# Optimization experiments

Measured on AMD Instinct MI355X. Metric: run time of the kernel, lower is better.

## Reference

```python
import jax, jax.numpy as jnp
import numpy as np

EPS = 1e-5  # torch LayerNorm default


def setup_inputs() -> dict:
    key = jax.random.key(0)
    ks = jax.random.split(key, 4)
    B, S, D = 8, 1024, 768
    return {
        "q": jax.random.normal(ks[0], (B, S, D), dtype=jnp.float32),
        "k": jax.random.normal(ks[1], (B, S, D), dtype=jnp.float32),
        "v": jax.random.normal(ks[2], (B, S, D), dtype=jnp.float32),
        "W": jax.random.normal(ks[3], (D, D), dtype=jnp.float32) * (1.0 / np.sqrt(D)),
        "gamma": jnp.ones((D,), dtype=jnp.float32),
        "beta": jnp.zeros((D,), dtype=jnp.float32),
        "n_heads": 12,
    }


def reference(q, k, v, W, gamma, beta, n_heads):
    # Shapes: q,k,v [B,S,D]; W [D,D] (torch Linear weight, y = x @ W.T)
    B, S, D = q.shape
    Dh = D // n_heads

    proj = lambda x: jax.nn.relu(x @ W.T)
    q1, k1, v1 = proj(q), proj(k), proj(v)

    # chunk(dim=2) + cat(dim=0) == reshape to per-head [B,S,H,Dh]
    split = lambda x: x.reshape(B, S, n_heads, Dh)
    qh, kh, vh = split(q1), split(k1), split(v1)

    scale = 1.0 / (Dh ** 0.5)
    scores = jnp.einsum("bqhd,bkhd->bhqk", qh, kh) * scale  # [B,H,S,S]
    attn = jax.nn.softmax(scores, axis=-1)  # dropout is identity in eval mode
    out = jnp.einsum("bhqk,bkhd->bqhd", attn, vh).reshape(B, S, D)

    # `outputs += outputs + q` in torch -> outputs = 2*outputs + q
    out = 2.0 * out + q

    mu = jnp.mean(out, axis=-1, keepdims=True)
    var = jnp.var(out, axis=-1, keepdims=True)
    return (out - mu) / jnp.sqrt(var + EPS) * gamma + beta
```

## Files before the change

kernel.cpp:

```cpp
#include <hip/hip_runtime.h>
#include <hip/hip_bf16.h>

#define B_  8
#define S_  1024
#define D_  768
#define H_  12
#define DH_ 64

typedef __attribute__((ext_vector_type(8))) short bf16x8;
typedef __attribute__((ext_vector_type(4))) float f32x4;
typedef __attribute__((ext_vector_type(16))) float f32x16;

__device__ inline short f2bf(float f) {
    unsigned u = __builtin_bit_cast(unsigned, f);
    u = (u + 0x7fffu + ((u >> 16) & 1u)) >> 16;
    return (short)u;
}
__device__ inline float exp2_fast(float x) {
    float r; asm("v_exp_f32 %0, %1" : "=v"(r) : "v"(x)); return r;
}
__device__ inline unsigned cvt_pk_bf16(float lo, float hi) {
    unsigned r; asm("v_cvt_pk_bf16_f32 %0, %1, %2" : "=v"(r) : "v"(lo), "v"(hi)); return r;
}
__device__ inline float rcp_fast(float x) {
    float r; asm("v_rcp_f32 %0, %1" : "=v"(r) : "v"(x)); return r;
}
__device__ inline void plswap(unsigned& a, unsigned& b) {
    auto r = __builtin_amdgcn_permlane32_swap(a, b, false, false);
    a = r[0]; b = r[1];
}
__device__ inline float2 xhalves(float x) {
    unsigned u = __builtin_bit_cast(unsigned, x);
    auto r = __builtin_amdgcn_permlane32_swap(u, u, false, false);
    return make_float2(__builtin_bit_cast(float, r[0]),
                       __builtin_bit_cast(float, r[1]));
}
__device__ inline void gl_lds16(const void* gsrc, char* ldst) {
    __builtin_amdgcn_global_load_lds(
        (const __attribute__((address_space(1))) unsigned int*)gsrc,
        (__attribute__((address_space(3))) unsigned int*)ldst,
        16, 0, 0);
}

__global__ __launch_bounds__(256) void convw_kernel(
    const float* __restrict__ W, short* __restrict__ Wb)
{
    int i = (blockIdx.x * 256 + threadIdx.x) * 8;
    f32x4 a = *(const f32x4*)(W + i);
    f32x4 b = *(const f32x4*)(W + i + 4);
    uint4 pk;
    pk.x = cvt_pk_bf16(a[0], a[1]); pk.y = cvt_pk_bf16(a[2], a[3]);
    pk.z = cvt_pk_bf16(b[0], b[1]); pk.w = cvt_pk_bf16(b[2], b[3]);
    *(uint4*)(Wb + i) = pk;
}

__global__ __launch_bounds__(512) void proj_kernel(
    const float* __restrict__ q, const float* __restrict__ k,
    const float* __restrict__ v, const short* __restrict__ Wb,
    short* __restrict__ q1, short* __restrict__ k1, short* __restrict__ v1t)
{
    __shared__ __align__(16) char lds[65536];

    int p  = blockIdx.x;
    int L  = (p & 7) * 96 + (p >> 3);
    int mt = L >> 1, nb = L & 1;
    int t  = mt >> 7;
    int m0 = (mt & 127) << 6;
    int n0 = nb * 384;
    const float* X = (t == 0) ? q : (t == 1) ? k : v;

    int tid = threadIdx.x, lane = tid & 63, w = tid >> 6;
    int l15 = lane & 15, g = lane >> 4;

    int xrow = w * 8 + (lane >> 3), xc = lane & 7;
    const float* xsrc = X + (size_t)(m0 + xrow) * D_ + ((xc ^ (xrow & 7)) << 2);
    char* xdst = lds + w * 1024;
    int wrow0 = w * 48 + (lane >> 2), wc = lane & 3;
    int wrow1 = wrow0 + 16, wrow2 = wrow0 + 32;
    const short* wsrc0 = Wb + (size_t)(n0 + wrow0) * D_ + ((wc ^ ((wrow0 >> 1) & 3)) << 3);
    const short* wsrc1 = Wb + (size_t)(n0 + wrow1) * D_ + ((wc ^ ((wrow1 >> 1) & 3)) << 3);
    const short* wsrc2 = Wb + (size_t)(n0 + wrow2) * D_ + ((wc ^ ((wrow2 >> 1) & 3)) << 3);
    char* wdst = lds + 16384 + w * 3072;

#define ISSUE(s_, b_) do { int _ko = (s_) * 32; \
        gl_lds16(xsrc + _ko, xdst + (b_) * 8192); \
        gl_lds16(wsrc0 + _ko, wdst + (b_) * 24576); \
        gl_lds16(wsrc1 + _ko, wdst + (b_) * 24576 + 1024); \
        gl_lds16(wsrc2 + _ko, wdst + (b_) * 24576 + 2048); \
    } while (0)

    f32x4 acc[4][3];
    #pragma unroll
    for (int m = 0; m < 4; m++)
        #pragma unroll
        for (int n = 0; n < 3; n++) acc[m][n] = (f32x4){0.f, 0.f, 0.f, 0.f};

    ISSUE(0, 0);
    for (int s = 0; s < 24; ++s) {
        __builtin_amdgcn_s_barrier();
        asm volatile("" ::: "memory");
        if (s + 1 < 24) {
            ISSUE(s + 1, (s + 1) & 1);
            asm volatile("s_waitcnt vmcnt(4)" ::: "memory");
        } else {
            asm volatile("s_waitcnt vmcnt(0)" ::: "memory");
        }
        __builtin_amdgcn_s_barrier();
        asm volatile("" ::: "memory");

        const char* Xb = lds + (s & 1) * 8192;
        const char* Wp = lds + 16384 + (s & 1) * 24576;
        bf16x8 af[4];
        #pragma unroll
        for (int m = 0; m < 4; m++) {
            int r = m * 16 + l15;
            const char* rp = Xb + r * 128;
            f32x4 lo = *(const f32x4*)(rp + (((2 * g)     ^ (r & 7)) << 4));
            f32x4 hi = *(const f32x4*)(rp + (((2 * g + 1) ^ (r & 7)) << 4));
            uint4 pk;
            pk.x = cvt_pk_bf16(lo[0], lo[1]); pk.y = cvt_pk_bf16(lo[2], lo[3]);
            pk.z = cvt_pk_bf16(hi[0], hi[1]); pk.w = cvt_pk_bf16(hi[2], hi[3]);
            af[m] = __builtin_bit_cast(bf16x8, pk);
        }
        bf16x8 bfv[3];
        #pragma unroll
        for (int n = 0; n < 3; n++) {
            int r = w * 48 + n * 16 + l15;
            bfv[n] = *(const bf16x8*)(Wp + r * 64 + ((g ^ ((r >> 1) & 3)) << 4));
        }
        __builtin_amdgcn_s_setprio(1);
        #pragma unroll
        for (int m = 0; m < 4; m++)
            #pragma unroll
            for (int n = 0; n < 3; n++)
                acc[m][n] = __builtin_amdgcn_mfma_f32_16x16x32_bf16(
                    af[m], bfv[n], acc[m][n], 0, 0, 0);
        __builtin_amdgcn_s_setprio(0);
    }
#undef ISSUE

    __syncthreads();
    const float sc1 = (t == 1) ? 0.18033688011112793f : 1.0f;
    #pragma unroll
    for (int m = 0; m < 4; m++)
        #pragma unroll
        for (int n = 0; n < 3; n++)
            #pragma unroll
            for (int r = 0; r < 4; r++) {
                int row = m * 16 + g * 4 + r;
                int col = w * 48 + n * 16 + l15;
                short vv = f2bf(fmaxf(acc[m][n][r], 0.f) * sc1);
                if (t == 2)
                    *(short*)(lds + col * 128 + (((row >> 3) ^ (col & 7)) << 4)
                              + ((row & 7) << 1)) = vv;
                else
                    *(short*)(lds + row * 768 + (((col >> 3) ^ (row & 7)) << 4)
                              + ((col & 7) << 1)) = vv;
            }
    __syncthreads();
    int bb2 = m0 >> 10;
    if (t == 2) {
        #pragma unroll
        for (int j = 0; j < 6; j++) {
            int c = tid * 6 + j;
            int vr = c >> 3, ch = c & 7;
            bf16x8 val = *(const bf16x8*)(lds + vr * 128 + ((ch ^ (vr & 7)) << 4));
            int gc = n0 + vr, h = gc >> 6, dh = gc & 63;
            *(bf16x8*)(v1t + (((size_t)bb2 * H_ + h) * DH_ + dh) * S_
                       + (m0 & 1023) + ch * 8) = val;
        }
    } else {
        short* dst0 = t ? k1 : q1;
        #pragma unroll
        for (int j = 0; j < 6; j++) {
            int c = tid * 6 + j;
            int row = c / 48, ch = c % 48;
            bf16x8 val = *(const bf16x8*)(lds + row * 768 + ((ch ^ (row & 7)) << 4));
            int m = m0 + row, ss = m & 1023;
            int gc = n0 + ch * 8, h = gc >> 6, dh = gc & 63;
            *(bf16x8*)(dst0 + (((size_t)bb2 * H_ + h) * S_ + ss) * DH_ + dh) = val;
        }
    }
}

__global__ __launch_bounds__(256, 3) void attn_kernel(
    const short* __restrict__ q1, const short* __restrict__ k1,
    const short* __restrict__ v1t, float* __restrict__ out)
{
    __shared__ short Klds[2][4096];
    __shared__ short Vlds[2][4096];
    __shared__ float lsum_lds[4][32];

    int d    = blockIdx.x;
    int head = (d & 7) + ((d >> 6) << 3);
    int qi   = (d >> 3) & 7;
    int bb   = head / H_, hh = head % H_;

    int tid = threadIdx.x, lane = tid & 63, w = tid >> 6;
    int l31 = lane & 31, hi = lane >> 5;
    int qbase = (qi * 4 + w) * 32;

    const short* Qp = q1  + (size_t)head * S_ * DH_;
    const short* Kp = k1  + (size_t)head * S_ * DH_;
    const short* Vp = v1t + (size_t)head * DH_ * S_;

    int sr = tid >> 2, sc = tid & 3;
    int swz0 = sr * 128 + ((sc       ^ (sr & 7)) << 4);
    int swz1 = sr * 128 + (((sc + 4) ^ (sr & 7)) << 4);

    bf16x8 stK0, stK1, stV0, stV1;

#define LOADST(kvb) do { \
        const short* _kg = Kp + (size_t)((kvb) + sr) * DH_; \
        const short* _vg = Vp + (size_t)sr * S_ + (kvb); \
        stK0 = *(const bf16x8*)(_kg + sc * 8); \
        stK1 = *(const bf16x8*)(_kg + (sc + 4) * 8); \
        stV0 = *(const bf16x8*)(_vg + sc * 8); \
        stV1 = *(const bf16x8*)(_vg + (sc + 4) * 8); \
    } while (0)
#define WRITEST(buf) do { \
        char* _kb = (char*)&Klds[buf][0]; \
        char* _vb = (char*)&Vlds[buf][0]; \
        *(bf16x8*)(_kb + swz0) = stK0; \
        *(bf16x8*)(_kb + swz1) = stK1; \
        *(bf16x8*)(_vb + swz0) = stV0; \
        *(bf16x8*)(_vb + swz1) = stV1; \
    } while (0)

    bf16x8 qf[4];
    #pragma unroll
    for (int kb = 0; kb < 4; kb++)
        qf[kb] = *(const bf16x8*)(Qp + (size_t)(qbase + l31) * DH_ + kb * 16 + hi * 8);

    f32x16 o0, o1;
    #pragma unroll
    for (int r = 0; r < 16; r++) { o0[r] = 0.f; o1[r] = 0.f; }
    float mreg = -1e30f, lsum = 0.f;

    int xk = l31 & 7;

    auto subtile = [&](int cur, int j) {
        const char* Kt = (const char*)&Klds[cur][0];
        const char* Vt = (const char*)&Vlds[cur][0];
        int rK = (32 * j + l31) * 128;
        bf16x8 kf0 = *(const bf16x8*)(Kt + rK + (((0 + hi) ^ xk) << 4));
        bf16x8 kf1 = *(const bf16x8*)(Kt + rK + (((2 + hi) ^ xk) << 4));
        bf16x8 kf2 = *(const bf16x8*)(Kt + rK + (((4 + hi) ^ xk) << 4));
        bf16x8 kf3 = *(const bf16x8*)(Kt + rK + (((6 + hi) ^ xk) << 4));
        int rV0 = l31 * 128, rV1 = (32 + l31) * 128;
        int s0 = ((4 * j + hi) ^ xk) << 4, s1 = ((4 * j + 2 + hi) ^ xk) << 4;
        bf16x8 vf00 = *(const bf16x8*)(Vt + rV0 + s0);
        bf16x8 vf01 = *(const bf16x8*)(Vt + rV0 + s1);
        bf16x8 vf10 = *(const bf16x8*)(Vt + rV1 + s0);
        bf16x8 vf11 = *(const bf16x8*)(Vt + rV1 + s1);

        f32x16 s;
        #pragma unroll
        for (int r = 0; r < 16; r++) s[r] = 0.f;
        __builtin_amdgcn_s_setprio(1);
        s = __builtin_amdgcn_mfma_f32_32x32x16_bf16(kf0, qf[0], s, 0, 0, 0);
        s = __builtin_amdgcn_mfma_f32_32x32x16_bf16(kf1, qf[1], s, 0, 0, 0);
        s = __builtin_amdgcn_mfma_f32_32x32x16_bf16(kf2, qf[2], s, 0, 0, 0);
        s = __builtin_amdgcn_mfma_f32_32x32x16_bf16(kf3, qf[3], s, 0, 0, 0);
        __builtin_amdgcn_s_setprio(0);

        float t0 = fmaxf(s[0], s[1]),   t1 = fmaxf(s[2], s[3]);
        float t2 = fmaxf(s[4], s[5]),   t3 = fmaxf(s[6], s[7]);
        float t4 = fmaxf(s[8], s[9]),   t5 = fmaxf(s[10], s[11]);
        float t6 = fmaxf(s[12], s[13]), t7 = fmaxf(s[14], s[15]);
        float u0 = fmaxf(t0, t1), u1 = fmaxf(t2, t3);
        float u2 = fmaxf(t4, t5), u3 = fmaxf(t6, t7);
        float pmax = fmaxf(fmaxf(u0, u1), fmaxf(u2, u3));
        float2 ph = xhalves(pmax);
        pmax = fmaxf(ph.x, ph.y);

        if (!__all(pmax <= mreg + 8.f)) {
            float mn = fmaxf(mreg, pmax);
            float sc_ = exp2_fast(mreg - mn);
            mreg = mn; lsum *= sc_;
            if (hi == 0) lsum_lds[w][l31] = sc_;
            asm volatile("s_waitcnt lgkmcnt(0)" ::: "memory");
            #pragma unroll
            for (int r = 0; r < 16; r++) {
                int crow = (r & 3) + ((r >> 2) << 3) + (hi << 2);
                float srw = lsum_lds[w][crow];
                o0[r] *= srw; o1[r] *= srw;
            }
        }

        #pragma unroll
        for (int r = 0; r < 16; r++) s[r] = exp2_fast(s[r] - mreg);

        float a0 = s[0] + s[1],   a1 = s[2] + s[3];
        float a2 = s[4] + s[5],   a3 = s[6] + s[7];
        float a4 = s[8] + s[9],   a5 = s[10] + s[11];
        float a6 = s[12] + s[13], a7 = s[14] + s[15];
        float rsum = ((a0 + a1) + (a2 + a3)) + ((a4 + a5) + (a6 + a7));
        float2 rh = xhalves(rsum);
        lsum += rh.x + rh.y;

        unsigned c0 = cvt_pk_bf16(s[0], s[1]);
        unsigned c1 = cvt_pk_bf16(s[2], s[3]);
        unsigned c2 = cvt_pk_bf16(s[4], s[5]);
        unsigned c3 = cvt_pk_bf16(s[6], s[7]);
        unsigned c4 = cvt_pk_bf16(s[8], s[9]);
        unsigned c5 = cvt_pk_bf16(s[10], s[11]);
        unsigned c6 = cvt_pk_bf16(s[12], s[13]);
        unsigned c7 = cvt_pk_bf16(s[14], s[15]);
        plswap(c0, c2);
        plswap(c1, c3);
        plswap(c4, c6);
        plswap(c5, c7);

        union U { unsigned u[4]; bf16x8 v; };
        U f0, f1;
        f0.u[0] = c0; f0.u[1] = c1; f0.u[2] = c2; f0.u[3] = c3;
        f1.u[0] = c4; f1.u[1] = c5; f1.u[2] = c6; f1.u[3] = c7;

        __builtin_amdgcn_s_setprio(1);
        o0 = __builtin_amdgcn_mfma_f32_32x32x16_bf16(f0.v, vf00, o0, 0, 0, 0);
        o0 = __builtin_amdgcn_mfma_f32_32x32x16_bf16(f1.v, vf01, o0, 0, 0, 0);
        o1 = __builtin_amdgcn_mfma_f32_32x32x16_bf16(f0.v, vf10, o1, 0, 0, 0);
        o1 = __builtin_amdgcn_mfma_f32_32x32x16_bf16(f1.v, vf11, o1, 0, 0, 0);
        __builtin_amdgcn_s_setprio(0);
    };

    LOADST(0);
    WRITEST(0);
    LOADST(64);
    asm volatile("s_waitcnt lgkmcnt(0)" ::: "memory");
    __builtin_amdgcn_s_barrier();
    asm volatile("" ::: "memory");

    int cur = 0;
    for (int t = 0; t < 16; t++) {
        if (t < 15) {
            WRITEST(cur ^ 1);
            if (t < 14) LOADST((t + 2) * 64);
        }
        subtile(cur, 0);
        subtile(cur, 1);
        if (t < 15) {
            asm volatile("" ::: "memory");
            asm volatile("s_waitcnt lgkmcnt(0)" ::: "memory");
            __builtin_amdgcn_s_barrier();
            asm volatile("" ::: "memory");
        }
        cur ^= 1;
    }
#undef LOADST
#undef WRITEST

    if (hi == 0) lsum_lds[w][l31] = lsum;
    asm volatile("s_waitcnt lgkmcnt(0)" ::: "memory");
    #pragma unroll
    for (int r = 0; r < 16; r++) {
        int crow = (r & 3) + ((r >> 2) << 3) + (hi << 2);
        float inv = rcp_fast(lsum_lds[w][crow]);
        float* op = out + ((size_t)(bb * S_ + qbase + crow)) * D_ + hh * DH_ + l31;
        op[0]  = o0[r] * inv;
        op[32] = o1[r] * inv;
    }
}

__global__ __launch_bounds__(192) void ln_kernel(
    const float* __restrict__ qin, const float* __restrict__ gamma,
    const float* __restrict__ beta, float* __restrict__ out)
{
    int row = blockIdx.x;
    int tid = threadIdx.x;
    size_t base = (size_t)row * D_ + tid * 4;

    f32x4 o  = *(const f32x4*)(out + base);
    f32x4 qv = *(const f32x4*)(qin + base);
    f32x4 x;
    float sum = 0.f, sq = 0.f;
    #pragma unroll
    for (int i = 0; i < 4; i++) {
        x[i] = 2.f * o[i] + qv[i];
        sum += x[i];
        sq  += x[i] * x[i];
    }
    #pragma unroll
    for (int msk = 1; msk < 64; msk <<= 1) {
        sum += __shfl_xor(sum, msk);
        sq  += __shfl_xor(sq, msk);
    }
    __shared__ float s1[3], s2[3];
    if ((tid & 63) == 0) { s1[tid >> 6] = sum; s2[tid >> 6] = sq; }
    __syncthreads();
    sum = s1[0] + s1[1] + s1[2];
    sq  = s2[0] + s2[1] + s2[2];
    float mu   = sum * (1.f / D_);
    float var  = sq * (1.f / D_) - mu * mu;
    float rstd = rsqrtf(var + 1e-5f);
    f32x4 g = *(const f32x4*)(gamma + tid * 4);
    f32x4 b = *(const f32x4*)(beta + tid * 4);
    f32x4 y;
    #pragma unroll
    for (int i = 0; i < 4; i++)
        y[i] = (x[i] - mu) * rstd * g[i] + b[i];
    *(f32x4*)(out + base) = y;
}

extern "C" void kernel_launch(void* const* d_in, const int* in_sizes, int n_in,
                              void* d_out, int out_size, void* d_ws, size_t ws_size,
                              hipStream_t stream)
{
    const float* q     = (const float*)d_in[0];
    const float* k     = (const float*)d_in[1];
    const float* v     = (const float*)d_in[2];
    const float* W     = (const float*)d_in[3];
    const float* gamma = (const float*)d_in[4];
    const float* beta  = (const float*)d_in[5];

    size_t per = (size_t)B_ * H_ * S_ * DH_;
    short* q1  = (short*)d_ws;
    short* k1  = q1 + per;
    short* v1t = k1 + per;
    short* Wb  = v1t + per;
    float* out = (float*)d_out;

    convw_kernel<<<dim3(288), dim3(256), 0, stream>>>(W, Wb);
    proj_kernel<<<dim3(768), dim3(512), 0, stream>>>(q, k, v, Wb, q1, k1, v1t);
    attn_kernel<<<dim3(768), dim3(256), 0, stream>>>(q1, k1, v1t, out);
    ln_kernel<<<dim3(B_ * S_), dim3(192), 0, stream>>>(q, gamma, beta, out);
}
```

Measured before the change: 117.5 us.

## Retile projection GEMM to 128x256 tiles with register-staged bf16 A conversion

The projection GEMM moves from 64x384 tiles with 512 threads to 128x256 tiles with 256 threads, where each wave computes a 64x128 sub-tile (4x8 MFMA accumulators). The fp32 activations are now loaded into registers one step ahead, converted to bf16 once, and written to LDS. Previously every k-step read fp32 from LDS and converted it inside the MFMA loop. The loop uses a single barrier per iteration. The aim is more MFMA work per LDS read, less conversion work, and fewer barriers, at the cost of more accumulator registers and fewer blocks (576).

```diff
diff --git a/kernel.cpp b/kernel.cpp
--- a/kernel.cpp
+++ b/kernel.cpp
@@ -54,7 +54,7 @@
     *(uint4*)(Wb + i) = pk;
 }
 
-__global__ __launch_bounds__(512) void proj_kernel(
+__global__ __launch_bounds__(256) void proj_kernel(
     const float* __restrict__ q, const float* __restrict__ k,
     const float* __restrict__ v, const short* __restrict__ Wb,
     short* __restrict__ q1, short* __restrict__ k1, short* __restrict__ v1t)
@@ -62,122 +62,145 @@
     __shared__ __align__(16) char lds[65536];
 
     int p  = blockIdx.x;
-    int L  = (p & 7) * 96 + (p >> 3);
-    int mt = L >> 1, nb = L & 1;
-    int t  = mt >> 7;
-    int m0 = (mt & 127) << 6;
-    int n0 = nb * 384;
+    int L  = (p & 7) * 72 + (p >> 3);
+    int mt = L / 3, nt = L % 3;
+    int t  = mt >> 6;
+    int m0 = (mt & 63) << 7;
+    int n0 = nt << 8;
     const float* X = (t == 0) ? q : (t == 1) ? k : v;
 
     int tid = threadIdx.x, lane = tid & 63, w = tid >> 6;
+    int wr = w >> 1, wc = w & 1;
     int l15 = lane & 15, g = lane >> 4;
 
-    int xrow = w * 8 + (lane >> 3), xc = lane & 7;
-    const float* xsrc = X + (size_t)(m0 + xrow) * D_ + ((xc ^ (xrow & 7)) << 2);
-    char* xdst = lds + w * 1024;
-    int wrow0 = w * 48 + (lane >> 2), wc = lane & 3;
-    int wrow1 = wrow0 + 16, wrow2 = wrow0 + 32;
-    const short* wsrc0 = Wb + (size_t)(n0 + wrow0) * D_ + ((wc ^ ((wrow0 >> 1) & 3)) << 3);
-    const short* wsrc1 = Wb + (size_t)(n0 + wrow1) * D_ + ((wc ^ ((wrow1 >> 1) & 3)) << 3);
-    const short* wsrc2 = Wb + (size_t)(n0 + wrow2) * D_ + ((wc ^ ((wrow2 >> 1) & 3)) << 3);
-    char* wdst = lds + 16384 + w * 3072;
-
-#define ISSUE(s_, b_) do { int _ko = (s_) * 32; \
-        gl_lds16(xsrc + _ko, xdst + (b_) * 8192); \
-        gl_lds16(wsrc0 + _ko, wdst + (b_) * 24576); \
-        gl_lds16(wsrc1 + _ko, wdst + (b_) * 24576 + 1024); \
-        gl_lds16(wsrc2 + _ko, wdst + (b_) * 24576 + 2048); \
+    int tr = tid >> 1, ch = tid & 1;
+    const float* asrc = X + (size_t)(m0 + tr) * D_ + ch * 16;
+    int awb0 = tr * 64 + (((2 * ch)     ^ ((tr >> 1) & 3)) << 4);
+    int awb1 = tr * 64 + (((2 * ch + 1) ^ ((tr >> 1) & 3)) << 4);
+
+    const short* bsrc[4];
+    int bofs[4];
+    #pragma unroll
+    for (int i = 0; i < 4; i++) {
+        int r = w * 64 + i * 16 + (lane >> 2);
+        int c = lane & 3;
+        bsrc[i] = Wb + (size_t)(n0 + r) * D_ + ((c ^ ((r >> 1) & 3)) << 3);
+        bofs[i] = (w * 64 + i * 16) * 64;
+    }
+
+    f32x4 pf[4];
+#define LOADA(s_) do { \
+        pf[0] = *(const f32x4*)(asrc + (s_) * 32); \
+        pf[1] = *(const f32x4*)(asrc + (s_) * 32 + 4); \
+        pf[2] = *(const f32x4*)(asrc + (s_) * 32 + 8); \
+        pf[3] = *(const f32x4*)(asrc + (s_) * 32 + 12); \
     } while (0)
-
-    f32x4 acc[4][3];
+#define ISSUE_B(s_, b_) do { \
+        _Pragma("unroll") \
+        for (int i = 0; i < 4; i++) \
+            gl_lds16(bsrc[i] + (s_) * 32, lds + (b_) * 24576 + 8192 + bofs[i]); \
+    } while (0)
+#define CVT_WRITE_A(b_) do { \
+        uint4 u0, u1; \
+        u0.x = cvt_pk_bf16(pf[0][0], pf[0][1]); u0.y = cvt_pk_bf16(pf[0][2], pf[0][3]); \
+        u0.z = cvt_pk_bf16(pf[1][0], pf[1][1]); u0.w = cvt_pk_bf16(pf[1][2], pf[1][3]); \
+        u1.x = cvt_pk_bf16(pf[2][0], pf[2][1]); u1.y = cvt_pk_bf16(pf[2][2], pf[2][3]); \
+        u1.z = cvt_pk_bf16(pf[3][0], pf[3][1]); u1.w = cvt_pk_bf16(pf[3][2], pf[3][3]); \
+        *(uint4*)(lds + (b_) * 24576 + awb0) = u0; \
+        *(uint4*)(lds + (b_) * 24576 + awb1) = u1; \
+    } while (0)
+
+    f32x4 acc[4][8];
     #pragma unroll
     for (int m = 0; m < 4; m++)
         #pragma unroll
-        for (int n = 0; n < 3; n++) acc[m][n] = (f32x4){0.f, 0.f, 0.f, 0.f};
-
-    ISSUE(0, 0);
+        for (int n = 0; n < 8; n++) acc[m][n] = (f32x4){0.f, 0.f, 0.f, 0.f};
+
+    LOADA(0);
+    ISSUE_B(0, 0);
+    CVT_WRITE_A(0);
+    LOADA(1);
+    asm volatile("s_waitcnt vmcnt(4) lgkmcnt(0)" ::: "memory");
+    __builtin_amdgcn_s_barrier();
+    asm volatile("" ::: "memory");
+
+    #pragma unroll 2
     for (int s = 0; s < 24; ++s) {
-        __builtin_amdgcn_s_barrier();
-        asm volatile("" ::: "memory");
+        const char* Ab = lds + (s & 1) * 24576;
+        const char* Bb = Ab + 8192;
+        bf16x8 af[4];
+        #pragma unroll
+        for (int m = 0; m < 4; m++) {
+            int ra = wr * 64 + m * 16 + l15;
+            af[m] = *(const bf16x8*)(Ab + ra * 64 + ((g ^ ((ra >> 1) & 3)) << 4));
+        }
+        __builtin_amdgcn_s_setprio(1);
+        #pragma unroll
+        for (int n = 0; n < 8; n++) {
+            int rb = wc * 128 + n * 16 + l15;
+            bf16x8 bv = *(const bf16x8*)(Bb + rb * 64 + ((g ^ ((rb >> 1) & 3)) << 4));
+            #pragma unroll
+            for (int m = 0; m < 4; m++)
+                acc[m][n] = __builtin_amdgcn_mfma_f32_16x16x32_bf16(
+                    af[m], bv, acc[m][n], 0, 0, 0);
+        }
+        __builtin_amdgcn_s_setprio(0);
+
         if (s + 1 < 24) {
-            ISSUE(s + 1, (s + 1) & 1);
-            asm volatile("s_waitcnt vmcnt(4)" ::: "memory");
-        } else {
-            asm volatile("s_waitcnt vmcnt(0)" ::: "memory");
-        }
-        __builtin_amdgcn_s_barrier();
-        asm volatile("" ::: "memory");
-
-        const char* Xb = lds + (s & 1) * 8192;
-        const char* Wp = lds + 16384 + (s & 1) * 24576;
-        bf16x8 af[4];
-        #pragma unroll
-        for (int m = 0; m < 4; m++) {
-            int r = m * 16 + l15;
-            const char* rp = Xb + r * 128;
-            f32x4 lo = *(const f32x4*)(rp + (((2 * g)     ^ (r & 7)) << 4));
-            f32x4 hi = *(const f32x4*)(rp + (((2 * g + 1) ^ (r & 7)) << 4));
-            uint4 pk;
-            pk.x = cvt_pk_bf16(lo[0], lo[1]); pk.y = cvt_pk_bf16(lo[2], lo[3]);
-            pk.z = cvt_pk_bf16(hi[0], hi[1]); pk.w = cvt_pk_bf16(hi[2], hi[3]);
-            af[m] = __builtin_bit_cast(bf16x8, pk);
-        }
-        bf16x8 bfv[3];
-        #pragma unroll
-        for (int n = 0; n < 3; n++) {
-            int r = w * 48 + n * 16 + l15;
-            bfv[n] = *(const bf16x8*)(Wp + r * 64 + ((g ^ ((r >> 1) & 3)) << 4));
-        }
-        __builtin_amdgcn_s_setprio(1);
-        #pragma unroll
-        for (int m = 0; m < 4; m++)
-            #pragma unroll
-            for (int n = 0; n < 3; n++)
-                acc[m][n] = __builtin_amdgcn_mfma_f32_16x16x32_bf16(
-                    af[m], bfv[n], acc[m][n], 0, 0, 0);
-        __builtin_amdgcn_s_setprio(0);
-    }
-#undef ISSUE
+            ISSUE_B(s + 1, (s + 1) & 1);
+            CVT_WRITE_A((s + 1) & 1);
+            if (s + 2 < 24) {
+                LOADA(s + 2);
+                asm volatile("s_waitcnt vmcnt(4) lgkmcnt(0)" ::: "memory");
+            } else {
+                asm volatile("s_waitcnt vmcnt(0) lgkmcnt(0)" ::: "memory");
+            }
+            __builtin_amdgcn_s_barrier();
+            asm volatile("" ::: "memory");
+        }
+    }
+#undef LOADA
+#undef ISSUE_B
+#undef CVT_WRITE_A
 
     __syncthreads();
     const float sc1 = (t == 1) ? 0.18033688011112793f : 1.0f;
     #pragma unroll
     for (int m = 0; m < 4; m++)
         #pragma unroll
-        for (int n = 0; n < 3; n++)
+        for (int n = 0; n < 8; n++)
             #pragma unroll
             for (int r = 0; r < 4; r++) {
-                int row = m * 16 + g * 4 + r;
-                int col = w * 48 + n * 16 + l15;
+                int row = wr * 64 + m * 16 + g * 4 + r;
+                int col = wc * 128 + n * 16 + l15;
                 short vv = f2bf(fmaxf(acc[m][n][r], 0.f) * sc1);
                 if (t == 2)
-                    *(short*)(lds + col * 128 + (((row >> 3) ^ (col & 7)) << 4)
+                    *(short*)(lds + col * 256 + (((row >> 3) ^ (col & 15)) << 4)
                               + ((row & 7) << 1)) = vv;
                 else
-                    *(short*)(lds + row * 768 + (((col >> 3) ^ (row & 7)) << 4)
+                    *(short*)(lds + row * 512 + (((col >> 3) ^ (row & 31)) << 4)
                               + ((col & 7) << 1)) = vv;
             }
     __syncthreads();
     int bb2 = m0 >> 10;
     if (t == 2) {
-        #pragma unroll
-        for (int j = 0; j < 6; j++) {
-            int c = tid * 6 + j;
-            int vr = c >> 3, ch = c & 7;
-            bf16x8 val = *(const bf16x8*)(lds + vr * 128 + ((ch ^ (vr & 7)) << 4));
-            int gc = n0 + vr, h = gc >> 6, dh = gc & 63;
-            *(bf16x8*)(v1t + (((size_t)bb2 * H_ + h) * DH_ + dh) * S_
-                       + (m0 & 1023) + ch * 8) = val;
+        int col = tid;
+        int gc = n0 + col, h = gc >> 6, dh = gc & 63;
+        short* dst = v1t + (((size_t)bb2 * H_ + h) * DH_ + dh) * S_ + (m0 & 1023);
+        #pragma unroll
+        for (int j = 0; j < 16; j++) {
+            bf16x8 val = *(const bf16x8*)(lds + col * 256 + ((j ^ (col & 15)) << 4));
+            *(bf16x8*)(dst + j * 8) = val;
         }
     } else {
-        short* dst0 = t ? k1 : q1;
-        #pragma unroll
-        for (int j = 0; j < 6; j++) {
-            int c = tid * 6 + j;
-            int row = c / 48, ch = c % 48;
-            bf16x8 val = *(const bf16x8*)(lds + row * 768 + ((ch ^ (row & 7)) << 4));
-            int m = m0 + row, ss = m & 1023;
-            int gc = n0 + ch * 8, h = gc >> 6, dh = gc & 63;
+        int row = tid >> 1, c0 = (tid & 1) << 4;
+        int m = m0 + row, ss = m & 1023;
+        short* dst0 = (t ? k1 : q1);
+        #pragma unroll
+        for (int j = 0; j < 16; j++) {
+            int cc = c0 + j;
+            bf16x8 val = *(const bf16x8*)(lds + row * 512 + ((cc ^ (row & 31)) << 4));
+            int gc = n0 + cc * 8, h = gc >> 6, dh = gc & 63;
             *(bf16x8*)(dst0 + (((size_t)bb2 * H_ + h) * S_ + ss) * DH_ + dh) = val;
         }
     }
@@ -422,7 +445,7 @@
     float* out = (float*)d_out;
 
     convw_kernel<<<dim3(288), dim3(256), 0, stream>>>(W, Wb);
-    proj_kernel<<<dim3(768), dim3(512), 0, stream>>>(q, k, v, Wb, q1, k1, v1t);
+    proj_kernel<<<dim3(576), dim3(256), 0, stream>>>(q, k, v, Wb, q1, k1, v1t);
     attn_kernel<<<dim3(768), dim3(256), 0, stream>>>(q1, k1, v1t, out);
     ln_kernel<<<dim3(B_ * S_), dim3(192), 0, stream>>>(q, gamma, beta, out);
 }
```

Measured after the change: 164.6 us. +40.0%, slower.

## Fuse q/k/v projections into one block sharing each W tile

Applied to the files above, without the earlier changes.

Each projection block now computes the q, k and v projections for the same 64-row tile at once. The W tile in LDS and the bf16 B-fragments are loaded once and reused across all three inputs, cutting W traffic and the block count from 768 to 256. In exchange LDS use per block grows to 96KB and the accumulator registers triple, which lowers occupancy. With 256 blocks on a large GPU the grid may also underfill the compute units.

```diff
diff --git a/kernel.cpp b/kernel.cpp
--- a/kernel.cpp
+++ b/kernel.cpp
@@ -59,41 +59,45 @@
     const float* __restrict__ v, const short* __restrict__ Wb,
     short* __restrict__ q1, short* __restrict__ k1, short* __restrict__ v1t)
 {
-    __shared__ __align__(16) char lds[65536];
+    __shared__ __align__(16) char lds[98304];
 
     int p  = blockIdx.x;
-    int L  = (p & 7) * 96 + (p >> 3);
+    int L  = (p & 7) * 32 + (p >> 3);
     int mt = L >> 1, nb = L & 1;
-    int t  = mt >> 7;
-    int m0 = (mt & 127) << 6;
+    int m0 = mt << 6;
     int n0 = nb * 384;
-    const float* X = (t == 0) ? q : (t == 1) ? k : v;
 
     int tid = threadIdx.x, lane = tid & 63, w = tid >> 6;
     int l15 = lane & 15, g = lane >> 4;
 
     int xrow = w * 8 + (lane >> 3), xc = lane & 7;
-    const float* xsrc = X + (size_t)(m0 + xrow) * D_ + ((xc ^ (xrow & 7)) << 2);
-    char* xdst = lds + w * 1024;
+    size_t xoff = (size_t)(m0 + xrow) * D_ + ((xc ^ (xrow & 7)) << 2);
+    const float* xs0 = q + xoff;
+    const float* xs1 = k + xoff;
+    const float* xs2 = v + xoff;
     int wrow0 = w * 48 + (lane >> 2), wc = lane & 3;
     int wrow1 = wrow0 + 16, wrow2 = wrow0 + 32;
     const short* wsrc0 = Wb + (size_t)(n0 + wrow0) * D_ + ((wc ^ ((wrow0 >> 1) & 3)) << 3);
     const short* wsrc1 = Wb + (size_t)(n0 + wrow1) * D_ + ((wc ^ ((wrow1 >> 1) & 3)) << 3);
     const short* wsrc2 = Wb + (size_t)(n0 + wrow2) * D_ + ((wc ^ ((wrow2 >> 1) & 3)) << 3);
-    char* wdst = lds + 16384 + w * 3072;
 
 #define ISSUE(s_, b_) do { int _ko = (s_) * 32; \
-        gl_lds16(xsrc + _ko, xdst + (b_) * 8192); \
-        gl_lds16(wsrc0 + _ko, wdst + (b_) * 24576); \
-        gl_lds16(wsrc1 + _ko, wdst + (b_) * 24576 + 1024); \
-        gl_lds16(wsrc2 + _ko, wdst + (b_) * 24576 + 2048); \
+        char* _bb = lds + (b_) * 49152; \
+        gl_lds16(xs0 + _ko, _bb + w * 1024); \
+        gl_lds16(xs1 + _ko, _bb + 8192 + w * 1024); \
+        gl_lds16(xs2 + _ko, _bb + 16384 + w * 1024); \
+        gl_lds16(wsrc0 + _ko, _bb + 24576 + w * 3072); \
+        gl_lds16(wsrc1 + _ko, _bb + 24576 + w * 3072 + 1024); \
+        gl_lds16(wsrc2 + _ko, _bb + 24576 + w * 3072 + 2048); \
     } while (0)
 
-    f32x4 acc[4][3];
-    #pragma unroll
-    for (int m = 0; m < 4; m++)
-        #pragma unroll
-        for (int n = 0; n < 3; n++) acc[m][n] = (f32x4){0.f, 0.f, 0.f, 0.f};
+    f32x4 acc[3][4][3];
+    #pragma unroll
+    for (int t = 0; t < 3; t++)
+        #pragma unroll
+        for (int m = 0; m < 4; m++)
+            #pragma unroll
+            for (int n = 0; n < 3; n++) acc[t][m][n] = (f32x4){0.f, 0.f, 0.f, 0.f};
 
     ISSUE(0, 0);
     for (int s = 0; s < 24; ++s) {
@@ -101,84 +105,91 @@
         asm volatile("" ::: "memory");
         if (s + 1 < 24) {
             ISSUE(s + 1, (s + 1) & 1);
-            asm volatile("s_waitcnt vmcnt(4)" ::: "memory");
+            asm volatile("s_waitcnt vmcnt(6)" ::: "memory");
         } else {
             asm volatile("s_waitcnt vmcnt(0)" ::: "memory");
         }
         __builtin_amdgcn_s_barrier();
         asm volatile("" ::: "memory");
 
-        const char* Xb = lds + (s & 1) * 8192;
-        const char* Wp = lds + 16384 + (s & 1) * 24576;
-        bf16x8 af[4];
-        #pragma unroll
-        for (int m = 0; m < 4; m++) {
-            int r = m * 16 + l15;
-            const char* rp = Xb + r * 128;
-            f32x4 lo = *(const f32x4*)(rp + (((2 * g)     ^ (r & 7)) << 4));
-            f32x4 hi = *(const f32x4*)(rp + (((2 * g + 1) ^ (r & 7)) << 4));
-            uint4 pk;
-            pk.x = cvt_pk_bf16(lo[0], lo[1]); pk.y = cvt_pk_bf16(lo[2], lo[3]);
-            pk.z = cvt_pk_bf16(hi[0], hi[1]); pk.w = cvt_pk_bf16(hi[2], hi[3]);
-            af[m] = __builtin_bit_cast(bf16x8, pk);
-        }
+        const char* bb = lds + (s & 1) * 49152;
+        const char* Wp = bb + 24576;
         bf16x8 bfv[3];
         #pragma unroll
         for (int n = 0; n < 3; n++) {
             int r = w * 48 + n * 16 + l15;
             bfv[n] = *(const bf16x8*)(Wp + r * 64 + ((g ^ ((r >> 1) & 3)) << 4));
         }
-        __builtin_amdgcn_s_setprio(1);
+        #pragma unroll
+        for (int t = 0; t < 3; t++) {
+            const char* Xb = bb + t * 8192;
+            bf16x8 af[4];
+            #pragma unroll
+            for (int m = 0; m < 4; m++) {
+                int r = m * 16 + l15;
+                const char* rp = Xb + r * 128;
+                f32x4 lo = *(const f32x4*)(rp + (((2 * g)     ^ (r & 7)) << 4));
+                f32x4 hi = *(const f32x4*)(rp + (((2 * g + 1) ^ (r & 7)) << 4));
+                uint4 pk;
+                pk.x = cvt_pk_bf16(lo[0], lo[1]); pk.y = cvt_pk_bf16(lo[2], lo[3]);
+                pk.z = cvt_pk_bf16(hi[0], hi[1]); pk.w = cvt_pk_bf16(hi[2], hi[3]);
+                af[m] = __builtin_bit_cast(bf16x8, pk);
+            }
+            __builtin_amdgcn_s_setprio(1);
+            #pragma unroll
+            for (int m = 0; m < 4; m++)
+                #pragma unroll
+                for (int n = 0; n < 3; n++)
+                    acc[t][m][n] = __builtin_amdgcn_mfma_f32_16x16x32_bf16(
+                        af[m], bfv[n], acc[t][m][n], 0, 0, 0);
+            __builtin_amdgcn_s_setprio(0);
+        }
+    }
+#undef ISSUE
+
+    int bb2 = m0 >> 10;
+    #pragma unroll
+    for (int t = 0; t < 3; t++) {
+        __syncthreads();
+        const float sc1 = (t == 1) ? 0.18033688011112793f : 1.0f;
         #pragma unroll
         for (int m = 0; m < 4; m++)
             #pragma unroll
             for (int n = 0; n < 3; n++)
-                acc[m][n] = __builtin_amdgcn_mfma_f32_16x16x32_bf16(
-                    af[m], bfv[n], acc[m][n], 0, 0, 0);
-        __builtin_amdgcn_s_setprio(0);
-    }
-#undef ISSUE
-
-    __syncthreads();
-    const float sc1 = (t == 1) ? 0.18033688011112793f : 1.0f;
-    #pragma unroll
-    for (int m = 0; m < 4; m++)
-        #pragma unroll
-        for (int n = 0; n < 3; n++)
-            #pragma unroll
-            for (int r = 0; r < 4; r++) {
-                int row = m * 16 + g * 4 + r;
-                int col = w * 48 + n * 16 + l15;
-                short vv = f2bf(fmaxf(acc[m][n][r], 0.f) * sc1);
-                if (t == 2)
-                    *(short*)(lds + col * 128 + (((row >> 3) ^ (col & 7)) << 4)
-                              + ((row & 7) << 1)) = vv;
-                else
-                    *(short*)(lds + row * 768 + (((col >> 3) ^ (row & 7)) << 4)
-                              + ((col & 7) << 1)) = vv;
+                #pragma unroll
+                for (int r = 0; r < 4; r++) {
+                    int row = m * 16 + g * 4 + r;
+                    int col = w * 48 + n * 16 + l15;
+                    short vv = f2bf(fmaxf(acc[t][m][n][r], 0.f) * sc1);
+                    if (t == 2)
+                        *(short*)(lds + col * 128 + (((row >> 3) ^ (col & 7)) << 4)
+                                  + ((row & 7) << 1)) = vv;
+                    else
+                        *(short*)(lds + row * 768 + (((col >> 3) ^ (row & 7)) << 4)
+                                  + ((col & 7) << 1)) = vv;
+                }
+        __syncthreads();
+        if (t == 2) {
+            #pragma unroll
+            for (int j = 0; j < 6; j++) {
+                int c = tid * 6 + j;
+                int vr = c >> 3, ch = c & 7;
+                bf16x8 val = *(const bf16x8*)(lds + vr * 128 + ((ch ^ (vr & 7)) << 4));
+                int gc = n0 + vr, h = gc >> 6, dh = gc & 63;
+                *(bf16x8*)(v1t + (((size_t)bb2 * H_ + h) * DH_ + dh) * S_
+                           + (m0 & 1023) + ch * 8) = val;
             }
-    __syncthreads();
-    int bb2 = m0 >> 10;
-    if (t == 2) {
-        #pragma unroll
-        for (int j = 0; j < 6; j++) {
-            int c = tid * 6 + j;
-            int vr = c >> 3, ch = c & 7;
-            bf16x8 val = *(const bf16x8*)(lds + vr * 128 + ((ch ^ (vr & 7)) << 4));
-            int gc = n0 + vr, h = gc >> 6, dh = gc & 63;
-            *(bf16x8*)(v1t + (((size_t)bb2 * H_ + h) * DH_ + dh) * S_
-                       + (m0 & 1023) + ch * 8) = val;
-        }
-    } else {
-        short* dst0 = t ? k1 : q1;
-        #pragma unroll
-        for (int j = 0; j < 6; j++) {
-            int c = tid * 6 + j;
-            int row = c / 48, ch = c % 48;
-            bf16x8 val = *(const bf16x8*)(lds + row * 768 + ((ch ^ (row & 7)) << 4));
-            int m = m0 + row, ss = m & 1023;
-            int gc = n0 + ch * 8, h = gc >> 6, dh = gc & 63;
-            *(bf16x8*)(dst0 + (((size_t)bb2 * H_ + h) * S_ + ss) * DH_ + dh) = val;
+        } else {
+            short* dst0 = t ? k1 : q1;
+            #pragma unroll
+            for (int j = 0; j < 6; j++) {
+                int c = tid * 6 + j;
+                int row = c / 48, ch = c % 48;
+                bf16x8 val = *(const bf16x8*)(lds + row * 768 + ((ch ^ (row & 7)) << 4));
+                int m = m0 + row, ss = m & 1023;
+                int gc = n0 + ch * 8, h = gc >> 6, dh = gc & 63;
+                *(bf16x8*)(dst0 + (((size_t)bb2 * H_ + h) * S_ + ss) * DH_ + dh) = val;
+            }
         }
     }
 }
@@ -422,7 +433,7 @@
     float* out = (float*)d_out;
 
     convw_kernel<<<dim3(288), dim3(256), 0, stream>>>(W, Wb);
-    proj_kernel<<<dim3(768), dim3(512), 0, stream>>>(q, k, v, Wb, q1, k1, v1t);
+    proj_kernel<<<dim3(256), dim3(512), 0, stream>>>(q, k, v, Wb, q1, k1, v1t);
     attn_kernel<<<dim3(768), dim3(256), 0, stream>>>(q1, k1, v1t, out);
     ln_kernel<<<dim3(B_ * S_), dim3(192), 0, stream>>>(q, gamma, beta, out);
 }
```

Result: faster. 109.9 us, median of 3 (-6.5%).
